# Optimization experiments

Measured on AMD Instinct MI355X. Metric: run time of the kernel, lower is better.

## Reference

```python
import jax, jax.numpy as jnp
from jax import lax
import numpy as np

EPS = 1e-7          # BCE clamp
SMOOTH = 1.0        # Dice smoothing
INT_INF = jnp.int32(2**31 - 1)


def _bce_dice(p, t):
    """BCE + Dice loss (standard BCEDiceLoss): p, t float32 in [0,1]."""
    pc = jnp.clip(p, EPS, 1.0 - EPS)
    bce = -jnp.mean(t * jnp.log(pc) + (1.0 - t) * jnp.log1p(-pc))
    inter = jnp.sum(p * t)
    dice = 1.0 - (2.0 * inter + SMOOTH) / (jnp.sum(p) + jnp.sum(t) + SMOOTH)
    return bce + dice


def _ccl(mask):
    """4-connected component labeling per batch image.
    mask: [B,H,W] bool. Returns (labels, init_labels) int32; 0 = background.
    Iterative min-label propagation to a fixpoint (lax.while_loop)."""
    B, H, W = mask.shape
    init = jnp.where(mask, jnp.arange(1, B * H * W + 1, dtype=jnp.int32).reshape(B, H, W), 0)

    def step(lab):
        big = jnp.where(mask, lab, INT_INF)
        pad_h = jnp.full((B, 1, W), INT_INF, jnp.int32)
        pad_w = jnp.full((B, H, 1), INT_INF, jnp.int32)
        up    = jnp.concatenate([big[:, 1:, :], pad_h], axis=1)
        down  = jnp.concatenate([pad_h, big[:, :-1, :]], axis=1)
        left  = jnp.concatenate([big[:, :, 1:], pad_w], axis=2)
        right = jnp.concatenate([pad_w, big[:, :, :-1]], axis=2)
        m = jnp.minimum(big, jnp.minimum(jnp.minimum(up, down), jnp.minimum(left, right)))
        return jnp.where(mask, m, 0)

    def cond(c):
        return c[1]

    def body(c):
        new = step(c[0])
        return (new, jnp.any(new != c[0]))

    lab, _ = lax.while_loop(cond, body, (init, jnp.array(True)))
    return lab, init


def _forward(pred_out, target_mask, num_target_classes):
    f32 = jnp.float32
    B, C, H, W = pred_out.shape
    pred_masks = jnp.argmax(pred_out, axis=1)      # [B,H,W] int
    tm = target_mask[:, 0]                         # [B,H,W] int

    # background-vs-background BCEDice term
    res = _bce_dice((pred_masks == 0).astype(f32), (tm == 0).astype(f32))

    ph = jnp.zeros((B, H, W), f32)    # pred_placeholder
    pho = jnp.zeros((B, H, W), f32)   # pred_placeholder_out
    last_i = jnp.int32(1)

    # fixed loop over predicted classes (torch loops over unique values;
    # here: loop 1..C-1 gated by presence so absent classes are no-ops)
    for v in range(1, C):
        cur = pred_masks == v                       # class-v mask
        present = jnp.any(cur)
        lab, init = _ccl(cur)
        # number of connected components = pixels that kept their seed label
        n_comp = jnp.sum((lab == init) & cur).astype(jnp.int32)
        has_bg = jnp.any(~cur).astype(jnp.int32)    # 0 in cur_uniq?
        # sum_c (c_mask + last_i) over components == cur + n_comp*last_i everywhere
        inc = cur.astype(f32) + (n_comp * last_i).astype(f32)
        ph = jnp.where(present, ph + inc, ph)
        pho = jnp.where(cur, pred_out[:, v], pho)
        last_i = last_i + jnp.where(present, n_comp + has_bg, 0)

    # loop over nonzero target ids (bounded by num_target_classes), gated by presence
    for t in range(1, num_target_classes):
        target_m = tm == t
        present = jnp.any(target_m)
        n = jnp.sum(target_m)
        # torch.median(ph[target_m]): lower median of masked values
        vals = jnp.where(target_m.reshape(-1), ph.reshape(-1), jnp.inf)
        med = jnp.sort(vals)[jnp.maximum((n - 1) // 2, 0)]
        tm_f = target_m.astype(f32)
        contrib = _bce_dice(pho * (ph == med).astype(f32), tm_f)
        extra = jnp.sum(pho * ((ph != med) & target_m).astype(f32)) / jnp.maximum(n, 1).astype(f32)
        res = res + jnp.where(present, contrib + extra, 0.0)

    # len(torch.unique(target_mask)) with values in [0, num_target_classes)
    n_unique = jnp.sum(jnp.stack([jnp.any(tm == t) for t in range(num_target_classes)]).astype(jnp.int32))
    return res / (2 * n_unique + 1).astype(f32)


def setup_inputs() -> dict:
    key = jax.random.key(0)
    k1, k2 = jax.random.split(key)
    B, C, H, W = 8, 5, 768, 768
    pred_out = jax.random.uniform(k1, (B, C, H, W), dtype=jnp.float32)
    target_mask = jax.random.randint(k2, (B, 1, H, W), 0, 4, dtype=jnp.int32)
    return {"pred_out": pred_out, "target_mask": target_mask, "num_target_classes": 4}


def reference(pred_out, target_mask, num_target_classes):
    return _forward(pred_out, target_mask, num_target_classes)
```

## Files before the change

kernel.cpp:

```cpp
#include <hip/hip_runtime.h>
#include <stdint.h>
#include <math.h>

#define B_ 8
#define C_ 5
#define H_ 768
#define W_ 768
#define HW_ (H_*W_)
#define HWq (HW_/4)
#define NPIX (B_*HW_)
#define TB 8
#define INVAL 0xFFFFFFFFu
#define LN2F 0.69314718056f
#define BIASF 16.2f
#define TILE 32
#define TPR 24
#define TPC 24
#define NTILES (B_*TPR*TPC)
#define NPT 128
#define NNODES (NTILES*NPT)
#define SEAMS_PER_IMG (23*768)
#define NB_HALF (B_*SEAMS_PER_IMG)
#define NB_TOT (2*NB_HALF)
#define SEAMBLK (NB_TOT/256)
#define NCOPY 16

typedef unsigned long long ull;

static __device__ __forceinline__ unsigned pload(const unsigned* P, unsigned i) {
  return __hip_atomic_load(&P[i], __ATOMIC_RELAXED, __HIP_MEMORY_SCOPE_AGENT);
}
static __device__ unsigned findRootG(unsigned* P, unsigned i) {
  unsigned p = pload(P, i);
  if (p == i) return i;
  unsigned gp = pload(P, p);
  while (p != gp) {
    __hip_atomic_store(&P[i], gp, __ATOMIC_RELAXED, __HIP_MEMORY_SCOPE_AGENT);
    i = p; p = gp; gp = pload(P, p);
  }
  return p;
}
static __device__ bool uniteG(unsigned* P, unsigned a, unsigned b) {
  a = findRootG(P, a);
  b = findRootG(P, b);
  while (a != b) {
    if (a < b) { unsigned t = a; a = b; b = t; }
    unsigned old = atomicCAS(&P[a], a, b);
    if (old == a) return true;
    a = findRootG(P, old);
    b = findRootG(P, b);
  }
  return false;
}
static __device__ __forceinline__ unsigned ploadL(const unsigned* P, unsigned i) {
  return __hip_atomic_load(&P[i], __ATOMIC_RELAXED, __HIP_MEMORY_SCOPE_WORKGROUP);
}
static __device__ unsigned findRootL(const unsigned* P, unsigned i) {
  unsigned p = ploadL(P, i) & 0xFFFFu;
  while (p != i) { i = p; p = ploadL(P, i) & 0xFFFFu; }
  return i;
}
static __device__ void uniteL(unsigned* P, unsigned a, unsigned b) {
  a = findRootL(P, a);
  b = findRootL(P, b);
  while (a != b) {
    if (a < b) { unsigned t = a; a = b; b = t; }
    unsigned old = atomicCAS(&P[a], 0xFFFF0000u | a, 0xFFFF0000u | b);
    if (old == (0xFFFF0000u | a)) return;
    a = findRootL(P, old & 0xFFFFu);
    b = findRootL(P, b);
  }
}

__global__ __launch_bounds__(256, 8) void k_stats_ccl(
    const float* __restrict__ pred, const int* __restrict__ tgt,
    unsigned short* __restrict__ border, unsigned* __restrict__ P2,
    unsigned* __restrict__ rootcnt, double* __restrict__ sp)
{
  __shared__ ull h[NCOPY][41];
  __shared__ unsigned lab[TILE*TILE];
  __shared__ unsigned lclsw[TILE*TILE/4];
  __shared__ unsigned s_rt[4];
  unsigned char* lcls = (unsigned char*)lclsw;

  for (int i = threadIdx.x; i < NCOPY*41; i += 256) (&h[0][0])[i] = 0ull;
  if (threadIdx.x < 4) s_rt[threadIdx.x] = 0u;
  if (threadIdx.x < NPT) {
    unsigned n = (unsigned)blockIdx.x * NPT + threadIdx.x;
    P2[n] = n;
  }
  __syncthreads();

  const int cp = threadIdx.x & (NCOPY - 1);
  int blk = blockIdx.x;
  int b = blk / (TPR*TPC);
  int rem = blk - b * (TPR*TPC);
  int trow = rem / TPR;
  int ty0 = trow * TILE;
  int tx0 = (rem - trow * TPR) * TILE;

  unsigned pk = 0u;
  {
    const int baseq = ty0 * (W_/4) + (tx0 >> 2);
    const int qrow = threadIdx.x >> 3, qcol = threadIdx.x & 7;
    const int o = qrow * (W_/4) + qcol;
    const float4* pp = (const float4*)pred + (size_t)b * (C_*HWq) + baseq + o;
    float4 a0 = pp[0];
    float4 a1 = pp[HWq];
    float4 a2 = pp[2*HWq];
    float4 a3 = pp[3*HWq];
    float4 a4 = pp[4*HWq];
    int4 t4 = ((const int4*)tgt)[(size_t)b * HWq + baseq + o];
#pragma unroll
    for (int j = 0; j < 4; ++j) {
      float v0 = ((const float*)&a0)[j];
      float v1 = ((const float*)&a1)[j];
      float v2 = ((const float*)&a2)[j];
      float v3 = ((const float*)&a3)[j];
      float v4 = ((const float*)&a4)[j];
      int tt = ((const int*)&t4)[j];
      float best = v0; int bc = 0;
      if (v1 > best) { best = v1; bc = 1; }
      if (v2 > best) { best = v2; bc = 2; }
      if (v3 > best) { best = v3; bc = 3; }
      if (v4 > best) { best = v4; bc = 4; }
      unsigned tu = (unsigned)tt; if (tu >= TB) tu = TB - 1;
      ull w;
      if (bc) {
        float pc = fminf(fmaxf(best, 1e-7f), 1.0f - 1e-7f);
        float l2p = __log2f(pc);
        float l2m = __log2f(1.0f - pc);
        float logit = (l2p - l2m) * LN2F;
        float mag   = -l2m * LN2F;
        w = (1ull << 57)
          | ((ull)__float2uint_rn(best * 4096.0f) << 38)
          | ((ull)__float2uint_rn((logit + BIASF) * 64.0f) << 20)
          | (ull)__float2uint_rn(mag * 64.0f);
      } else {
        w = 1ull << 57;
      }
      atomicAdd(&h[cp][(int)tu * C_ + bc], w);
      pk |= ((unsigned)bc) << (8 * j);
    }
    lclsw[threadIdx.x] = pk;
  }
  __syncthreads();

  const int r = threadIdx.x >> 3, sub = threadIdx.x & 7;
  const int seg = r * TILE + sub * 4;
  unsigned Dw = (r < TILE-1) ? lclsw[threadIdx.x + 8] : 0u;
  unsigned rb = (sub < 7) ? (lclsw[threadIdx.x + 1] & 255u) : 0u;
  {
    uint4 lw;
    unsigned* lp = (unsigned*)&lw;
#pragma unroll
    for (int k = 0; k < 4; ++k) {
      int li = seg + k;
      unsigned c = (pk >> (8 * k)) & 255u;
      lp[k] = c ? (0xFFFF0000u | (unsigned)li) : INVAL;
    }
    *(uint4*)&lab[seg] = lw;
  }
  __syncthreads();

#pragma unroll
  for (int j = 0; j < 4; ++j) {
    unsigned c = (pk >> (8 * j)) & 255u;
    if (!c) continue;
    int li = seg + j;
    unsigned cr = (j < 3) ? ((pk >> (8 * (j + 1))) & 255u) : rb;
    if (cr == c) uniteL(lab, li, li + 1);
    if (((Dw >> (8 * j)) & 255u) == c) uniteL(lab, li, li + TILE);
  }
  __syncthreads();

  {
    uint4 lw = *(const uint4*)&lab[seg];
    const unsigned* lp = (const unsigned*)&lw;
#pragma unroll
    for (int k = 0; k < 4; ++k) {
      int li = seg + k;
      unsigned c = (pk >> (8 * k)) & 255u;
      if (c && (lp[k] & 0xFFFFu) == (unsigned)li) atomicAdd(&s_rt[c - 1], 1u);
    }
  }
  unsigned bc_c = 0, bc_rt = 0;
  if (threadIdx.x < NPT) {
    int bp = threadIdx.x;
    int tx, ty;
    if (bp < 32)       { ty = 0;       tx = bp; }
    else if (bp < 64)  { ty = TILE-1;  tx = bp - 32; }
    else if (bp < 96)  { tx = 0;       ty = bp - 64; }
    else               { tx = TILE-1;  ty = bp - 96; }
    int li = ty * TILE + tx;
    bc_c = lcls[li];
    if (bc_c) {
      bc_rt = findRootL(lab, (unsigned)li);
      atomicMin(&lab[bc_rt], ((unsigned)threadIdx.x << 16) | bc_rt);
    }
  }
  __syncthreads();
  if (threadIdx.x < NPT) {
    unsigned sub2 = bc_c ? (lab[bc_rt] >> 16) : 0u;
    border[blk * NPT + threadIdx.x] = (unsigned short)((bc_c << 8) | sub2);
  }
  if (threadIdx.x < 4) rootcnt[blk * 4 + threadIdx.x] = s_rt[threadIdx.x];
  if (threadIdx.x < 160) {
    int slot = threadIdx.x >> 2, comp = threadIdx.x & 3;
    double s = 0.0;
#pragma unroll
    for (int cc = 0; cc < NCOPY; ++cc) {
      ull w = h[cc][slot];
      if (comp == 0)      s += (double)(w >> 57);
      else if (comp == 1) s += (double)((w >> 38) & 0x7FFFFull) * (1.0/4096.0);
      else if (comp == 2) s += (double)((w >> 20) & 0x3FFFFull) * (1.0/64.0);
      else                s += (double)(w & 0x1FFFFull) * (1.0/64.0);
    }
    sp[(size_t)blk * 160 + threadIdx.x] = s;
  }
}

__global__ __launch_bounds__(256) void k_seam(const unsigned short* __restrict__ border,
                                              unsigned* __restrict__ P2,
                                              unsigned* __restrict__ smcnt,
                                              const double* __restrict__ sp,
                                              double* __restrict__ spf)
{
  __shared__ unsigned s_sub[4];
  __shared__ double red[256];
  if (threadIdx.x < 4) s_sub[threadIdx.x] = 0u;
  __syncthreads();
  int idx = blockIdx.x * blockDim.x + threadIdx.x;
  if (idx < NB_TOT) {
    int tA, tB, pA, pB;
    if (idx < NB_HALF) {
      int b = idx / SEAMS_PER_IMG;
      int r = idx - b * SEAMS_PER_IMG;
      int seam = r / W_;
      int x = r - seam * W_;
      int tj = x >> 5, k = x & 31;
      tA = (b * TPC + seam) * TPR + tj;
      tB = tA + TPR;
      pA = tA * NPT + 32 + k;
      pB = tB * NPT + 0 + k;
    } else {
      int i2 = idx - NB_HALF;
      int b = i2 / SEAMS_PER_IMG;
      int r = i2 - b * SEAMS_PER_IMG;
      int seam = r / H_;
      int y = r - seam * H_;
      int ti = y >> 5, k = y & 31;
      tA = (b * TPC + ti) * TPR + seam;
      tB = tA + 1;
      pA = tA * NPT + 96 + k;
      pB = tB * NPT + 64 + k;
    }
    unsigned a16 = border[pA];
    unsigned b16 = border[pB];
    unsigned ca = a16 >> 8, cb = b16 >> 8;
    if (ca && ca == cb) {
      if (uniteG(P2, (unsigned)tA * NPT + (a16 & 255u),
                     (unsigned)tB * NPT + (b16 & 255u)))
        atomicAdd(&s_sub[ca - 1], 1u);
    }
  }
  __syncthreads();
  if (threadIdx.x < 4) smcnt[blockIdx.x * 4 + threadIdx.x] = s_sub[threadIdx.x];
  if (blockIdx.x < 160) {
    double s = 0.0;
    for (int j = threadIdx.x; j < NTILES; j += 256) s += sp[(size_t)j * 160 + blockIdx.x];
    red[threadIdx.x] = s;
    __syncthreads();
    for (int off = 128; off; off >>= 1) {
      if (threadIdx.x < off) red[threadIdx.x] += red[threadIdx.x + off];
      __syncthreads();
    }
    if (threadIdx.x == 0) spf[blockIdx.x] = red[0];
  }
}

#define SH_CNT(t,c)   shist[((t)*C_+(c))*4 + 0]
#define SH_PRED(t,c)  shist[((t)*C_+(c))*4 + 1]
#define SH_LRAW(t,c)  shist[((t)*C_+(c))*4 + 2]
#define SH_MAG(t,c)   shist[((t)*C_+(c))*4 + 3]
__global__ __launch_bounds__(256) void k_final(
    const double* __restrict__ spf, const unsigned* __restrict__ rootcnt,
    const unsigned* __restrict__ smcnt, const int* __restrict__ ntcp,
    float* __restrict__ out)
{
  __shared__ double shist[160];
  __shared__ double s_col[C_][3];
  __shared__ unsigned s_cnti[TB*C_];
  __shared__ unsigned s_ctot[C_];
  __shared__ unsigned s_nc[4], s_sm[4];
  __shared__ float s_ph[C_];
  __shared__ double s_term[TB];
  __shared__ int s_NT;
  __shared__ int s_nun;

  if (threadIdx.x < 4) { s_nc[threadIdx.x] = 0u; s_sm[threadIdx.x] = 0u; }
  if (threadIdx.x < TB) s_term[threadIdx.x] = 0.0;
  __syncthreads();
  if (threadIdx.x < 160) shist[threadIdx.x] = spf[threadIdx.x];
  {
    unsigned a = 0;
    for (int j = threadIdx.x; j < NTILES * 4; j += 256) a += rootcnt[j];
    if (a) atomicAdd(&s_nc[threadIdx.x & 3], a);
  }
  {
    unsigned a = 0;
    for (int j = threadIdx.x; j < SEAMBLK * 4; j += 256) a += smcnt[j];
    if (a) atomicAdd(&s_sm[threadIdx.x & 3], a);
  }
  if (threadIdx.x == 0) {
    int NT = ntcp[0];
    if (NT < 1) NT = 1;
    if (NT > TB) NT = TB;
    s_NT = NT;
  }
  __syncthreads();

  if (threadIdx.x < TB * C_) s_cnti[threadIdx.x] = (unsigned)llrint(shist[threadIdx.x * 4]);
  __syncthreads();

  if (threadIdx.x < C_) {
    int c = threadIdx.x;
    double sc = 0.0, sp2 = 0.0, sl = 0.0;
    unsigned ct = 0;
#pragma unroll
    for (int t = 0; t < TB; ++t) {
      sc += SH_CNT(t, c);
      sp2 += SH_PRED(t, c);
      sl += -SH_MAG(t, c);
      ct += s_cnti[t * C_ + c];
    }
    s_col[c][0] = sc; s_col[c][1] = sp2; s_col[c][2] = sl;
    s_ctot[c] = ct;
  }
  __syncthreads();

  if (threadIdx.x == 0) {
#pragma unroll
    for (int cc = 0; cc < C_; ++cc) {
      float ph = 0.0f;
      int li = 1;
#pragma unroll
      for (int v = 1; v < C_; ++v) {
        unsigned ncv = s_nc[v - 1] - s_sm[v - 1];
        if (s_ctot[v] > 0) {
          int prod = (int)(ncv * (unsigned)li);
          float sv = (float)prod;
          float inc = ((cc == v) ? 1.0f : 0.0f) + sv;
          ph = ph + inc;
          li = li + (int)ncv + ((s_ctot[v] < (unsigned)NPIX) ? 1 : 0);
        }
      }
      s_ph[cc] = ph;
    }
  }
  __syncthreads();

  const float EPSF = 1e-7f;
  const double L1 = (double)logf(1.0f - EPSF);
  const double M1 = (double)log1pf(-(1.0f - EPSF));
  const double L0 = (double)logf(EPSF);
  const double M0 = (double)log1pf(-EPSF);
  const double N = (double)NPIX;
  const double BIASD = (double)BIASF;
  const int NT = s_NT;

  if (threadIdx.x == 0) {
    double nt0 = 0;
#pragma unroll
    for (int c = 0; c < C_; ++c) nt0 += SH_CNT(0, c);
    double np1 = (double)s_ctot[0];
    double n11 = SH_CNT(0, 0);
    s_term[0] = -(n11*L1 + (nt0 - n11)*L0 + (np1 - n11)*M1 + (N - nt0 - np1 + n11)*M0) / N
                + 1.0 - (2.0*n11 + 1.0) / (np1 + nt0 + 1.0);
    int nun = 0;
    for (int t = 0; t < NT; ++t) {
      long long s = 0;
#pragma unroll
      for (int c = 0; c < C_; ++c) s += (long long)s_cnti[t * C_ + c];
      if (s) nun++;
    }
    s_nun = nun;
  } else if (threadIdx.x < (unsigned)NT) {
    int t = threadIdx.x;
    long long ntti = 0;
#pragma unroll
    for (int c = 0; c < C_; ++c) ntti += (long long)s_cnti[t * C_ + c];
    if (ntti != 0) {
      double ntt = 0;
#pragma unroll
      for (int c = 0; c < C_; ++c) ntt += SH_CNT(t, c);
      float ph0 = s_ph[0], ph1 = s_ph[1], ph2 = s_ph[2], ph3 = s_ph[3], ph4 = s_ph[4];
      float pht[C_] = {ph0, ph1, ph2, ph3, ph4};
      int idx[C_] = {0, 1, 2, 3, 4};
#pragma unroll
      for (int i = 1; i < C_; ++i)
        for (int j = i; j > 0 && pht[idx[j]] < pht[idx[j-1]]; --j) {
          int tmp = idx[j]; idx[j] = idx[j-1]; idx[j-1] = tmp;
        }
      long long k = (ntti - 1) / 2;
      float med = pht[idx[C_ - 1]];
      long long cum = 0;
#pragma unroll
      for (int i = 0; i < C_; ++i) {
        cum += (long long)s_cnti[t * C_ + idx[i]];
        if (cum > k) { med = pht[idx[i]]; break; }
      }
      double A = 0, Bt = 0, inter = 0, sum_p = 0, ex = 0, nfg_t = 0, nfg_all = 0;
#pragma unroll
      for (int c = 1; c < C_; ++c) {
        double cnt_tc = SH_CNT(t, c);
        double mag_tc = SH_MAG(t, c);
        double spred_tc = SH_PRED(t, c);
        if (pht[c] == med) {
          double logit = SH_LRAW(t, c) - BIASD * cnt_tc;
          A += logit - mag_tc;
          inter += spred_tc;
          nfg_t += cnt_tc;
          nfg_all += s_col[c][0];
          sum_p += s_col[c][1];
          Bt += s_col[c][2] - (-mag_tc);
        } else {
          ex += spred_tc;
        }
      }
      double bce  = -(A + Bt + (ntt - nfg_t)*L0 + (N - ntt - (nfg_all - nfg_t))*M0) / N;
      double dice = 1.0 - (2.0*inter + 1.0) / (sum_p + ntt + 1.0);
      s_term[t] = bce + dice + ex / ntt;
    }
  }
  __syncthreads();
  if (threadIdx.x == 0) {
    double res = 0.0;
#pragma unroll
    for (int t = 0; t < TB; ++t) res += s_term[t];
    out[0] = (float)(res / (double)(2 * s_nun + 1));
  }
}

extern "C" void kernel_launch(void* const* d_in, const int* in_sizes, int n_in,
                              void* d_out, int out_size, void* d_ws, size_t ws_size,
                              hipStream_t stream) {
  const float* pred = (const float*)d_in[0];
  const int* tgt = (const int*)d_in[1];
  const int* ntc = (const int*)d_in[2];
  float* out = (float*)d_out;
  char* ws = (char*)d_ws;
  size_t off = 0;
  double* sp = (double*)(ws + off);              off += (size_t)NTILES * 160 * 8;
  double* spf = (double*)(ws + off);             off += 160 * 8;
  unsigned* P2 = (unsigned*)(ws + off);          off += (size_t)NNODES * 4;
  unsigned short* border = (unsigned short*)(ws + off); off += (size_t)NTILES * NPT * 2;
  unsigned* rootcnt = (unsigned*)(ws + off);     off += (size_t)NTILES * 4 * 4;
  unsigned* smcnt = (unsigned*)(ws + off);       off += (size_t)SEAMBLK * 4 * 4;

  hipLaunchKernelGGL(k_stats_ccl, dim3(NTILES), dim3(256), 0, stream,
                     pred, tgt, border, P2, rootcnt, sp);
  hipLaunchKernelGGL(k_seam, dim3(SEAMBLK), dim3(256), 0, stream,
                     border, P2, smcnt, sp, spf);
  hipLaunchKernelGGL(k_final, dim3(1), dim3(256), 0, stream,
                     spf, rootcnt, smcnt, ntc, out);
}
```

Baseline: 190.9 us.

## Fuse seam and final kernels via last-block atomic counter; widen histogram copies

```diff
diff --git a/kernel.cpp b/kernel.cpp
--- a/kernel.cpp
+++ b/kernel.cpp
@@ -23,7 +23,7 @@
 #define NB_HALF (B_*SEAMS_PER_IMG)
 #define NB_TOT (2*NB_HALF)
 #define SEAMBLK (NB_TOT/256)
-#define NCOPY 16
+#define NCOPY 32
 
 typedef unsigned long long ull;
 
@@ -75,7 +75,8 @@
 __global__ __launch_bounds__(256, 8) void k_stats_ccl(
     const float* __restrict__ pred, const int* __restrict__ tgt,
     unsigned short* __restrict__ border, unsigned* __restrict__ P2,
-    unsigned* __restrict__ rootcnt, double* __restrict__ sp)
+    unsigned* __restrict__ rootcnt, double* __restrict__ sp,
+    unsigned* __restrict__ ctrl)
 {
   __shared__ ull h[NCOPY][41];
   __shared__ unsigned lab[TILE*TILE];
@@ -89,6 +90,7 @@
     unsigned n = (unsigned)blockIdx.x * NPT + threadIdx.x;
     P2[n] = n;
   }
+  if (blockIdx.x == 0 && threadIdx.x == 0) ctrl[8] = 0u;
   __syncthreads();
 
   const int cp = threadIdx.x & (NCOPY - 1);
@@ -220,18 +222,34 @@
   }
 }
 
-__global__ __launch_bounds__(256) void k_seam(const unsigned short* __restrict__ border,
-                                              unsigned* __restrict__ P2,
-                                              unsigned* __restrict__ smcnt,
-                                              const double* __restrict__ sp,
-                                              double* __restrict__ spf)
+#define SH_CNT(t,c)   shist[((t)*C_+(c))*4 + 0]
+#define SH_PRED(t,c)  shist[((t)*C_+(c))*4 + 1]
+#define SH_LRAW(t,c)  shist[((t)*C_+(c))*4 + 2]
+#define SH_MAG(t,c)   shist[((t)*C_+(c))*4 + 3]
+__global__ __launch_bounds__(256) void k_seam_final(
+    const unsigned short* __restrict__ border, unsigned* __restrict__ P2,
+    const double* __restrict__ sp, const unsigned* __restrict__ rootcnt,
+    unsigned* __restrict__ smcnt, ull* __restrict__ spf_u,
+    unsigned* __restrict__ ctrl, const int* __restrict__ ntcp,
+    float* __restrict__ out)
 {
   __shared__ unsigned s_sub[4];
   __shared__ double red[256];
+  __shared__ int s_last;
+  __shared__ double shist[160];
+  __shared__ double s_col[C_][3];
+  __shared__ unsigned s_cnti[TB*C_];
+  __shared__ unsigned s_ctot[C_];
+  __shared__ unsigned s_nc[4], s_smg[4];
+  __shared__ float s_ph[C_];
+  __shared__ double s_term[TB];
+  __shared__ int s_NT;
+  __shared__ int s_nun;
+
   if (threadIdx.x < 4) s_sub[threadIdx.x] = 0u;
   __syncthreads();
   int idx = blockIdx.x * blockDim.x + threadIdx.x;
-  if (idx < NB_TOT) {
+  {
     int tA, tB, pA, pB;
     if (idx < NB_HALF) {
       int b = idx / SEAMS_PER_IMG;
@@ -264,8 +282,6 @@
         atomicAdd(&s_sub[ca - 1], 1u);
     }
   }
-  __syncthreads();
-  if (threadIdx.x < 4) smcnt[blockIdx.x * 4 + threadIdx.x] = s_sub[threadIdx.x];
   if (blockIdx.x < 160) {
     double s = 0.0;
     for (int j = threadIdx.x; j < NTILES; j += 256) s += sp[(size_t)j * 160 + blockIdx.x];
@@ -275,43 +291,30 @@
       if (threadIdx.x < off) red[threadIdx.x] += red[threadIdx.x + off];
       __syncthreads();
     }
-    if (threadIdx.x == 0) spf[blockIdx.x] = red[0];
-  }
-}
-
-#define SH_CNT(t,c)   shist[((t)*C_+(c))*4 + 0]
-#define SH_PRED(t,c)  shist[((t)*C_+(c))*4 + 1]
-#define SH_LRAW(t,c)  shist[((t)*C_+(c))*4 + 2]
-#define SH_MAG(t,c)   shist[((t)*C_+(c))*4 + 3]
-__global__ __launch_bounds__(256) void k_final(
-    const double* __restrict__ spf, const unsigned* __restrict__ rootcnt,
-    const unsigned* __restrict__ smcnt, const int* __restrict__ ntcp,
-    float* __restrict__ out)
-{
-  __shared__ double shist[160];
-  __shared__ double s_col[C_][3];
-  __shared__ unsigned s_cnti[TB*C_];
-  __shared__ unsigned s_ctot[C_];
-  __shared__ unsigned s_nc[4], s_sm[4];
-  __shared__ float s_ph[C_];
-  __shared__ double s_term[TB];
-  __shared__ int s_NT;
-  __shared__ int s_nun;
-
-  if (threadIdx.x < 4) { s_nc[threadIdx.x] = 0u; s_sm[threadIdx.x] = 0u; }
+    if (threadIdx.x == 0)
+      __hip_atomic_store(&spf_u[blockIdx.x], (ull)__double_as_longlong(red[0]),
+                         __ATOMIC_RELAXED, __HIP_MEMORY_SCOPE_AGENT);
+  }
+  __syncthreads();
+  if (threadIdx.x < 4)
+    __hip_atomic_store(&smcnt[blockIdx.x * 4 + threadIdx.x], s_sub[threadIdx.x],
+                       __ATOMIC_RELAXED, __HIP_MEMORY_SCOPE_AGENT);
+  __syncthreads();
+  if (threadIdx.x == 0) {
+    unsigned old = __hip_atomic_fetch_add(&ctrl[8], 1u,
+                     __ATOMIC_RELAXED, __HIP_MEMORY_SCOPE_AGENT);
+    s_last = (old == (unsigned)(SEAMBLK - 1));
+  }
+  __syncthreads();
+  if (!s_last) return;
+
+  if (threadIdx.x < 160) {
+    ull u = __hip_atomic_load(&spf_u[threadIdx.x],
+              __ATOMIC_RELAXED, __HIP_MEMORY_SCOPE_AGENT);
+    shist[threadIdx.x] = __longlong_as_double((long long)u);
+  }
+  if (threadIdx.x < 4) { s_nc[threadIdx.x] = 0u; s_smg[threadIdx.x] = 0u; }
   if (threadIdx.x < TB) s_term[threadIdx.x] = 0.0;
-  __syncthreads();
-  if (threadIdx.x < 160) shist[threadIdx.x] = spf[threadIdx.x];
-  {
-    unsigned a = 0;
-    for (int j = threadIdx.x; j < NTILES * 4; j += 256) a += rootcnt[j];
-    if (a) atomicAdd(&s_nc[threadIdx.x & 3], a);
-  }
-  {
-    unsigned a = 0;
-    for (int j = threadIdx.x; j < SEAMBLK * 4; j += 256) a += smcnt[j];
-    if (a) atomicAdd(&s_sm[threadIdx.x & 3], a);
-  }
   if (threadIdx.x == 0) {
     int NT = ntcp[0];
     if (NT < 1) NT = 1;
@@ -319,6 +322,18 @@
     s_NT = NT;
   }
   __syncthreads();
+  {
+    unsigned a = 0;
+    for (int j = threadIdx.x; j < NTILES * 4; j += 256) a += rootcnt[j];
+    if (a) atomicAdd(&s_nc[threadIdx.x & 3], a);
+  }
+  {
+    unsigned a = 0;
+    for (int j = threadIdx.x; j < SEAMBLK * 4; j += 256)
+      a += __hip_atomic_load(&smcnt[j], __ATOMIC_RELAXED, __HIP_MEMORY_SCOPE_AGENT);
+    if (a) atomicAdd(&s_smg[threadIdx.x & 3], a);
+  }
+  __syncthreads();
 
   if (threadIdx.x < TB * C_) s_cnti[threadIdx.x] = (unsigned)llrint(shist[threadIdx.x * 4]);
   __syncthreads();
@@ -346,7 +361,7 @@
       int li = 1;
 #pragma unroll
       for (int v = 1; v < C_; ++v) {
-        unsigned ncv = s_nc[v - 1] - s_sm[v - 1];
+        unsigned ncv = s_nc[v - 1] - s_smg[v - 1];
         if (s_ctot[v] > 0) {
           int prod = (int)(ncv * (unsigned)li);
           float sv = (float)prod;
@@ -394,21 +409,20 @@
       double ntt = 0;
 #pragma unroll
       for (int c = 0; c < C_; ++c) ntt += SH_CNT(t, c);
-      float ph0 = s_ph[0], ph1 = s_ph[1], ph2 = s_ph[2], ph3 = s_ph[3], ph4 = s_ph[4];
-      float pht[C_] = {ph0, ph1, ph2, ph3, ph4};
-      int idx[C_] = {0, 1, 2, 3, 4};
+      float pht[C_] = {s_ph[0], s_ph[1], s_ph[2], s_ph[3], s_ph[4]};
+      int idx2[C_] = {0, 1, 2, 3, 4};
 #pragma unroll
       for (int i = 1; i < C_; ++i)
-        for (int j = i; j > 0 && pht[idx[j]] < pht[idx[j-1]]; --j) {
-          int tmp = idx[j]; idx[j] = idx[j-1]; idx[j-1] = tmp;
+        for (int j = i; j > 0 && pht[idx2[j]] < pht[idx2[j-1]]; --j) {
+          int tmp = idx2[j]; idx2[j] = idx2[j-1]; idx2[j-1] = tmp;
         }
       long long k = (ntti - 1) / 2;
-      float med = pht[idx[C_ - 1]];
+      float med = pht[idx2[C_ - 1]];
       long long cum = 0;
 #pragma unroll
       for (int i = 0; i < C_; ++i) {
-        cum += (long long)s_cnti[t * C_ + idx[i]];
-        if (cum > k) { med = pht[idx[i]]; break; }
+        cum += (long long)s_cnti[t * C_ + idx2[i]];
+        if (cum > k) { med = pht[idx2[i]]; break; }
       }
       double A = 0, Bt = 0, inter = 0, sum_p = 0, ex = 0, nfg_t = 0, nfg_all = 0;
 #pragma unroll
@@ -451,17 +465,16 @@
   float* out = (float*)d_out;
   char* ws = (char*)d_ws;
   size_t off = 0;
+  unsigned* ctrl = (unsigned*)(ws + off);        off += 16 * 4;
+  ull* spf_u = (ull*)(ws + off);                 off += 160 * 8;
   double* sp = (double*)(ws + off);              off += (size_t)NTILES * 160 * 8;
-  double* spf = (double*)(ws + off);             off += 160 * 8;
   unsigned* P2 = (unsigned*)(ws + off);          off += (size_t)NNODES * 4;
   unsigned short* border = (unsigned short*)(ws + off); off += (size_t)NTILES * NPT * 2;
   unsigned* rootcnt = (unsigned*)(ws + off);     off += (size_t)NTILES * 4 * 4;
   unsigned* smcnt = (unsigned*)(ws + off);       off += (size_t)SEAMBLK * 4 * 4;
 
   hipLaunchKernelGGL(k_stats_ccl, dim3(NTILES), dim3(256), 0, stream,
-                     pred, tgt, border, P2, rootcnt, sp);
-  hipLaunchKernelGGL(k_seam, dim3(SEAMBLK), dim3(256), 0, stream,
-                     border, P2, smcnt, sp, spf);
-  hipLaunchKernelGGL(k_final, dim3(1), dim3(256), 0, stream,
-                     spf, rootcnt, smcnt, ntc, out);
-}
+                     pred, tgt, border, P2, rootcnt, sp, ctrl);
+  hipLaunchKernelGGL(k_seam_final, dim3(SEAMBLK), dim3(256), 0, stream,
+                     border, P2, sp, rootcnt, smcnt, spf_u, ctrl, ntc, out);
+}
```

Result: slower. 211.4 us (+10.8%).
